# Kernel tuning notes

Measured on AMD Instinct MI355X. Metric: run time of the kernel, lower is better.

The kernel has to match this reference:

```python
import jax, jax.numpy as jnp
import numpy as np

B, D_INNER, D_STATE, DT_RANK = 1024, 2560, 16, 160


def setup_inputs() -> dict:
    key = jax.random.key(0)
    ks = jax.random.split(key, 9)
    s = lambda n: 1.0 / np.sqrt(n)
    return {
        "x": jax.random.normal(ks[0], (B, D_INNER), jnp.float32),
        "h": jax.random.normal(ks[1], (B, D_INNER, D_STATE), jnp.float32),
        "W_dt_low": jax.random.normal(ks[2], (DT_RANK, D_INNER), jnp.float32) * s(D_INNER),
        "W_dt": jax.random.normal(ks[3], (D_INNER, DT_RANK), jnp.float32) * s(DT_RANK),
        "b_dt": jax.random.normal(ks[4], (D_INNER,), jnp.float32),
        "W_B": jax.random.normal(ks[5], (D_STATE, D_INNER), jnp.float32) * s(D_INNER),
        "W_C": jax.random.normal(ks[6], (D_STATE, D_INNER), jnp.float32) * s(D_INNER),
        "A_log": jax.random.uniform(ks[7], (D_INNER, D_STATE), jnp.float32, 0.0, 1.0),
        "D": jax.random.normal(ks[8], (D_INNER,), jnp.float32),
    }


def reference(x, h, W_dt_low, W_dt, b_dt, W_B, W_C, A_log, D):
    # Single-token Mamba selective-scan step (decode).
    # dt projections: d_inner -> dt_rank -> d_inner, then softplus
    dt = jax.nn.softplus(jnp.einsum('bd,rd->br', x, W_dt_low) @ W_dt.T + b_dt)  # [B, D_INNER]
    Bt = jnp.einsum('bd,nd->bn', x, W_B)  # [B, D_STATE]
    Ct = jnp.einsum('bd,nd->bn', x, W_C)  # [B, D_STATE]
    A = -jnp.exp(A_log)                   # [D_INNER, D_STATE]
    delta_A = jnp.exp(dt[:, :, None] * A[None])                 # [B, D_INNER, D_STATE]
    delta_B_x = dt[:, :, None] * Bt[:, None, :] * x[:, :, None] # [B, D_INNER, D_STATE]
    h_new = delta_A * h + delta_B_x
    y = jnp.einsum('bdn,bn->bd', h_new, Ct) + D * x             # [B, D_INNER]
    return y
```

## Files before the change

kernel.cpp:

```cpp
#include <hip/hip_runtime.h>
#include <hip/hip_bf16.h>
#include <math.h>

#define B_SZ    1024
#define DI      2560
#define DS      16
#define DR      160
#define NPROJ   192

typedef __bf16 bf16x8 __attribute__((ext_vector_type(8)));
typedef float  f32x4  __attribute__((ext_vector_type(4)));

__global__ void __launch_bounds__(256) convert_kernel(
    const float* __restrict__ x, const float* __restrict__ Wdl,
    const float* __restrict__ WB, const float* __restrict__ WC,
    const float* __restrict__ Wdt, const float* __restrict__ A_log,
    __bf16* __restrict__ xb, __bf16* __restrict__ wcat,
    __bf16* __restrict__ wdtb, float* __restrict__ negA) {
  int i = blockIdx.x * 256 + threadIdx.x;
  const int NX   = B_SZ * DI;
  const int NWDL = DR * DI;
  const int NWB  = DS * DI;
  const int NWDT = DI * DR;
  const int NA   = DI * DS;
  if (i < NX)   { xb[i] = (__bf16)x[i]; return; }
  i -= NX;
  if (i < NWDL) { wcat[i] = (__bf16)Wdl[i]; return; }
  i -= NWDL;
  if (i < NWB)  { wcat[NWDL + i] = (__bf16)WB[i]; return; }
  i -= NWB;
  if (i < NWB)  { wcat[NWDL + NWB + i] = (__bf16)WC[i]; return; }
  i -= NWB;
  if (i < NWDT) { wdtb[i] = (__bf16)Wdt[i]; return; }
  i -= NWDT;
  if (i < NA)   { negA[i] = -__expf(A_log[i]); }
}

__global__ void __launch_bounds__(256) proj_kernel(
    const __bf16* __restrict__ xb, const __bf16* __restrict__ wcat,
    __bf16* __restrict__ dtlow, float* __restrict__ Bt, float* __restrict__ Ct) {
  int gw    = blockIdx.x * 4 + (threadIdx.x >> 6);
  int lane  = threadIdx.x & 63;
  int mtile = gw & 63;
  int ntile = gw >> 6;
  int b0 = mtile * 16, n0 = ntile * 16;
  int m = lane & 15, quad = lane >> 4;
  const __bf16* ap = xb   + (size_t)(b0 + m) * DI + quad * 8;
  const __bf16* bp = wcat + (size_t)(n0 + m) * DI + quad * 8;
  f32x4 acc = {0.f, 0.f, 0.f, 0.f};
  for (int k0 = 0; k0 < DI; k0 += 32) {
    bf16x8 a = *(const bf16x8*)(ap + k0);
    bf16x8 b = *(const bf16x8*)(bp + k0);
    acc = __builtin_amdgcn_mfma_f32_16x16x32_bf16(a, b, acc, 0, 0, 0);
  }
  int nn = n0 + m;
#pragma unroll
  for (int r = 0; r < 4; ++r) {
    int bb = b0 + quad * 4 + r;
    float v = acc[r];
    if (nn < DR)            dtlow[bb * DR + nn] = (__bf16)v;
    else if (nn < DR + DS)  Bt[bb * DS + (nn - DR)] = v;
    else                    Ct[bb * DS + (nn - DR - DS)] = v;
  }
}

__global__ void __launch_bounds__(256) dt_kernel(
    const __bf16* __restrict__ dtlow, const __bf16* __restrict__ wdtb,
    const float* __restrict__ b_dt, float* __restrict__ dt) {
  int gw    = blockIdx.x * 4 + (threadIdx.x >> 6);
  int lane  = threadIdx.x & 63;
  int mtile = gw & 63;
  int ntile = gw >> 6;
  int b0 = mtile * 16, d0 = ntile * 16;
  int m = lane & 15, quad = lane >> 4;
  const __bf16* ap = dtlow + (size_t)(b0 + m) * DR + quad * 8;
  const __bf16* bp = wdtb  + (size_t)(d0 + m) * DR + quad * 8;
  f32x4 acc = {0.f, 0.f, 0.f, 0.f};
#pragma unroll
  for (int k0 = 0; k0 < DR; k0 += 32) {
    bf16x8 a = *(const bf16x8*)(ap + k0);
    bf16x8 b = *(const bf16x8*)(bp + k0);
    acc = __builtin_amdgcn_mfma_f32_16x16x32_bf16(a, b, acc, 0, 0, 0);
  }
  int dd = d0 + m;
  float bias = b_dt[dd];
#pragma unroll
  for (int r = 0; r < 4; ++r) {
    int bb = b0 + quad * 4 + r;
    float z = acc[r] + bias;
    float sp = (z > 20.f) ? z : log1pf(__expf(z));
    dt[(size_t)bb * DI + dd] = sp;
  }
}

__global__ void __launch_bounds__(256) ssm_kernel(
    const float* __restrict__ x, const float* __restrict__ h,
    const float* __restrict__ dt, const float* __restrict__ negA,
    const float* __restrict__ Bt, const float* __restrict__ Ct,
    const float* __restrict__ Dp, float* __restrict__ y) {
  int e = blockIdx.x * 256 + threadIdx.x;
  int b = e / DI;
  int d = e - b * DI;
  float dtv = dt[e];
  float xv  = x[e];
  float dtl = dtv * 1.44269504f;
  float dxv = dtv * xv;
  const float4* h4 = (const float4*)(h    + (size_t)e * DS);
  const float4* a4 = (const float4*)(negA + (size_t)d * DS);
  const float4* b4 = (const float4*)(Bt   + (size_t)b * DS);
  const float4* c4 = (const float4*)(Ct   + (size_t)b * DS);
  float acc = 0.f;
#pragma unroll
  for (int j = 0; j < 4; ++j) {
    float4 hv = h4[j], av = a4[j], bv = b4[j], cv = c4[j];
    acc += (exp2f(av.x * dtl) * hv.x + bv.x * dxv) * cv.x;
    acc += (exp2f(av.y * dtl) * hv.y + bv.y * dxv) * cv.y;
    acc += (exp2f(av.z * dtl) * hv.z + bv.z * dxv) * cv.z;
    acc += (exp2f(av.w * dtl) * hv.w + bv.w * dxv) * cv.w;
  }
  y[e] = acc + Dp[d] * xv;
}

extern "C" void kernel_launch(void* const* d_in, const int* in_sizes, int n_in,
                              void* d_out, int out_size, void* d_ws, size_t ws_size,
                              hipStream_t stream) {
  const float* x     = (const float*)d_in[0];
  const float* h     = (const float*)d_in[1];
  const float* Wdl   = (const float*)d_in[2];
  const float* Wdt   = (const float*)d_in[3];
  const float* b_dt  = (const float*)d_in[4];
  const float* WB    = (const float*)d_in[5];
  const float* WC    = (const float*)d_in[6];
  const float* A_log = (const float*)d_in[7];
  const float* Dp    = (const float*)d_in[8];
  float* y = (float*)d_out;

  char* ws = (char*)d_ws;
  __bf16* xb    = (__bf16*)(ws);
  __bf16* wcat  = (__bf16*)(ws + 5242880);
  __bf16* wdtb  = (__bf16*)(ws + 6225920);
  float*  negA  = (float*) (ws + 7045120);
  __bf16* dtlow = (__bf16*)(ws + 7208960);
  float*  Bt    = (float*) (ws + 7536640);
  float*  Ct    = (float*) (ws + 7602176);
  float*  dt    = (float*) (ws + 7667712);
  if (ws_size < 18153472) return;

  convert_kernel<<<13920, 256, 0, stream>>>(x, Wdl, WB, WC, Wdt, A_log,
                                            xb, wcat, wdtb, negA);
  proj_kernel<<<192, 256, 0, stream>>>(xb, wcat, dtlow, Bt, Ct);
  dt_kernel<<<2560, 256, 0, stream>>>(dtlow, wdtb, b_dt, dt);
  ssm_kernel<<<10240, 256, 0, stream>>>(x, h, dt, negA, Bt, Ct, Dp, y);
}
```

Measured before the change: 292.1 us.

## Fuse dt projection with SSM update and spread projection across more blocks

Merges the dt GEMM (with softplus) into the SSM state-update kernel, so dt is consumed from registers and never written to or read back from a B×D_INNER global buffer, and one launch disappears. The projection kernel now runs one wave per block over 768 blocks to spread work across more CUs, and its K loop is unrolled. A is prescaled by log2(e) and hardware exp2/log2 intrinsics are used. In exchange, the fused kernel reads h with a strided per-thread pattern set by the MFMA tile layout, which may coalesce worse than the old linear indexing.

```diff
diff --git a/kernel.cpp b/kernel.cpp
--- a/kernel.cpp
+++ b/kernel.cpp
@@ -11,12 +11,30 @@
 typedef __bf16 bf16x8 __attribute__((ext_vector_type(8)));
 typedef float  f32x4  __attribute__((ext_vector_type(4)));
 
+__device__ __forceinline__ float fast_exp2(float x) {
+#if __has_builtin(__builtin_amdgcn_exp2f)
+  return __builtin_amdgcn_exp2f(x);
+#else
+  return exp2f(x);
+#endif
+}
+__device__ __forceinline__ float fast_log2(float x) {
+#if __has_builtin(__builtin_amdgcn_logf)
+  return __builtin_amdgcn_logf(x);
+#else
+  return log2f(x);
+#endif
+}
+
+#define LOG2E 1.44269504088896f
+#define LN2   0.693147180559945f
+
 __global__ void __launch_bounds__(256) convert_kernel(
     const float* __restrict__ x, const float* __restrict__ Wdl,
     const float* __restrict__ WB, const float* __restrict__ WC,
     const float* __restrict__ Wdt, const float* __restrict__ A_log,
     __bf16* __restrict__ xb, __bf16* __restrict__ wcat,
-    __bf16* __restrict__ wdtb, float* __restrict__ negA) {
+    __bf16* __restrict__ wdtb, float* __restrict__ negA2) {
   int i = blockIdx.x * 256 + threadIdx.x;
   const int NX   = B_SZ * DI;
   const int NWDL = DR * DI;
@@ -33,14 +51,14 @@
   i -= NWB;
   if (i < NWDT) { wdtb[i] = (__bf16)Wdt[i]; return; }
   i -= NWDT;
-  if (i < NA)   { negA[i] = -__expf(A_log[i]); }
+  if (i < NA)   { negA2[i] = -fast_exp2(A_log[i] * LOG2E) * LOG2E; }
 }
 
-__global__ void __launch_bounds__(256) proj_kernel(
+__global__ void __launch_bounds__(64) proj_kernel(
     const __bf16* __restrict__ xb, const __bf16* __restrict__ wcat,
     __bf16* __restrict__ dtlow, float* __restrict__ Bt, float* __restrict__ Ct) {
-  int gw    = blockIdx.x * 4 + (threadIdx.x >> 6);
-  int lane  = threadIdx.x & 63;
+  int gw    = blockIdx.x;
+  int lane  = threadIdx.x;
   int mtile = gw & 63;
   int ntile = gw >> 6;
   int b0 = mtile * 16, n0 = ntile * 16;
@@ -48,6 +66,7 @@
   const __bf16* ap = xb   + (size_t)(b0 + m) * DI + quad * 8;
   const __bf16* bp = wcat + (size_t)(n0 + m) * DI + quad * 8;
   f32x4 acc = {0.f, 0.f, 0.f, 0.f};
+#pragma unroll 4
   for (int k0 = 0; k0 < DI; k0 += 32) {
     bf16x8 a = *(const bf16x8*)(ap + k0);
     bf16x8 b = *(const bf16x8*)(bp + k0);
@@ -64,15 +83,19 @@
   }
 }
 
-__global__ void __launch_bounds__(256) dt_kernel(
+__global__ void __launch_bounds__(256) dtssm_kernel(
     const __bf16* __restrict__ dtlow, const __bf16* __restrict__ wdtb,
-    const float* __restrict__ b_dt, float* __restrict__ dt) {
+    const float* __restrict__ b_dt, const float* __restrict__ x,
+    const float* __restrict__ h, const float* __restrict__ negA2,
+    const float* __restrict__ Bt, const float* __restrict__ Ct,
+    const float* __restrict__ Dp, float* __restrict__ y) {
   int gw    = blockIdx.x * 4 + (threadIdx.x >> 6);
   int lane  = threadIdx.x & 63;
   int mtile = gw & 63;
   int ntile = gw >> 6;
   int b0 = mtile * 16, d0 = ntile * 16;
   int m = lane & 15, quad = lane >> 4;
+
   const __bf16* ap = dtlow + (size_t)(b0 + m) * DR + quad * 8;
   const __bf16* bp = wdtb  + (size_t)(d0 + m) * DR + quad * 8;
   f32x4 acc = {0.f, 0.f, 0.f, 0.f};
@@ -82,43 +105,38 @@
     bf16x8 b = *(const bf16x8*)(bp + k0);
     acc = __builtin_amdgcn_mfma_f32_16x16x32_bf16(a, b, acc, 0, 0, 0);
   }
+
   int dd = d0 + m;
   float bias = b_dt[dd];
+  float dv   = Dp[dd];
+  const float4* a4 = (const float4*)(negA2 + (size_t)dd * DS);
+  float4 av0 = a4[0], av1 = a4[1], av2 = a4[2], av3 = a4[3];
+
 #pragma unroll
   for (int r = 0; r < 4; ++r) {
     int bb = b0 + quad * 4 + r;
     float z = acc[r] + bias;
-    float sp = (z > 20.f) ? z : log1pf(__expf(z));
-    dt[(size_t)bb * DI + dd] = sp;
+    float t = fast_exp2(z * LOG2E);
+    float dt = (z > 80.f) ? z : fast_log2(1.f + t) * LN2;
+
+    size_t e = (size_t)bb * DI + dd;
+    float xv  = x[e];
+    float dxv = dt * xv;
+    const float4* h4 = (const float4*)(h  + e * DS);
+    const float4* b4 = (const float4*)(Bt + (size_t)bb * DS);
+    const float4* c4 = (const float4*)(Ct + (size_t)bb * DS);
+    float s = 0.f;
+#pragma unroll
+    for (int j = 0; j < 4; ++j) {
+      float4 hv = h4[j], bv = b4[j], cv = c4[j];
+      float4 avj = (j == 0) ? av0 : (j == 1) ? av1 : (j == 2) ? av2 : av3;
+      s += (fast_exp2(avj.x * dt) * hv.x + bv.x * dxv) * cv.x;
+      s += (fast_exp2(avj.y * dt) * hv.y + bv.y * dxv) * cv.y;
+      s += (fast_exp2(avj.z * dt) * hv.z + bv.z * dxv) * cv.z;
+      s += (fast_exp2(avj.w * dt) * hv.w + bv.w * dxv) * cv.w;
+    }
+    y[e] = s + dv * xv;
   }
-}
-
-__global__ void __launch_bounds__(256) ssm_kernel(
-    const float* __restrict__ x, const float* __restrict__ h,
-    const float* __restrict__ dt, const float* __restrict__ negA,
-    const float* __restrict__ Bt, const float* __restrict__ Ct,
-    const float* __restrict__ Dp, float* __restrict__ y) {
-  int e = blockIdx.x * 256 + threadIdx.x;
-  int b = e / DI;
-  int d = e - b * DI;
-  float dtv = dt[e];
-  float xv  = x[e];
-  float dtl = dtv * 1.44269504f;
-  float dxv = dtv * xv;
-  const float4* h4 = (const float4*)(h    + (size_t)e * DS);
-  const float4* a4 = (const float4*)(negA + (size_t)d * DS);
-  const float4* b4 = (const float4*)(Bt   + (size_t)b * DS);
-  const float4* c4 = (const float4*)(Ct   + (size_t)b * DS);
-  float acc = 0.f;
-#pragma unroll
-  for (int j = 0; j < 4; ++j) {
-    float4 hv = h4[j], av = a4[j], bv = b4[j], cv = c4[j];
-    acc += (exp2f(av.x * dtl) * hv.x + bv.x * dxv) * cv.x;
-    acc += (exp2f(av.y * dtl) * hv.y + bv.y * dxv) * cv.y;
-    acc += (exp2f(av.z * dtl) * hv.z + bv.z * dxv) * cv.z;
-    acc += (exp2f(av.w * dtl) * hv.w + bv.w * dxv) * cv.w;
-  }
-  y[e] = acc + Dp[d] * xv;
 }
 
 extern "C" void kernel_launch(void* const* d_in, const int* in_sizes, int n_in,
@@ -139,16 +157,15 @@
   __bf16* xb    = (__bf16*)(ws);
   __bf16* wcat  = (__bf16*)(ws + 5242880);
   __bf16* wdtb  = (__bf16*)(ws + 6225920);
-  float*  negA  = (float*) (ws + 7045120);
+  float*  negA2 = (float*) (ws + 7045120);
   __bf16* dtlow = (__bf16*)(ws + 7208960);
   float*  Bt    = (float*) (ws + 7536640);
   float*  Ct    = (float*) (ws + 7602176);
-  float*  dt    = (float*) (ws + 7667712);
-  if (ws_size < 18153472) return;
+  if (ws_size < 7667712) return;
 
   convert_kernel<<<13920, 256, 0, stream>>>(x, Wdl, WB, WC, Wdt, A_log,
-                                            xb, wcat, wdtb, negA);
-  proj_kernel<<<192, 256, 0, stream>>>(xb, wcat, dtlow, Bt, Ct);
-  dt_kernel<<<2560, 256, 0, stream>>>(dtlow, wdtb, b_dt, dt);
-  ssm_kernel<<<10240, 256, 0, stream>>>(x, h, dt, negA, Bt, Ct, Dp, y);
+                                            xb, wcat, wdtb, negA2);
+  proj_kernel<<<768, 64, 0, stream>>>(xb, wcat, dtlow, Bt, Ct);
+  dtssm_kernel<<<2560, 256, 0, stream>>>(dtlow, wdtb, b_dt, x, h, negA2,
+                                         Bt, Ct, Dp, y);
 }
```

Result: no change. 295.9 us (+1.3%).
